# Kernel tuning notes

Measured on AMD Instinct MI355X. Metric: run time of the kernel, lower is better.

## Reference

```python
import jax, jax.numpy as jnp
import numpy as np
import math

L = 4          # num_layers
NH = 8         # num_heads
EPS = 1e-5


def _mha(x, Wqkv, bqkv, Wo, bo):
    # x: (S, B, D). Faithful to torch nn.MultiheadAttention (eval mode).
    S, B, D = x.shape
    hd = D // NH
    qkv = jnp.einsum('sbd,ed->sbe', x, Wqkv) + bqkv            # (S,B,3D)
    q, k, v = jnp.split(qkv, 3, axis=-1)
    def heads(t):
        return t.reshape(S, B, NH, hd).transpose(1, 2, 0, 3)   # (B,H,S,hd)
    q, k, v = heads(q), heads(k), heads(v)
    scale = 1.0 / math.sqrt(hd)
    att = jax.nn.softmax(jnp.einsum('bhqd,bhkd->bhqk', q * scale, k), axis=-1)
    o = jnp.einsum('bhqk,bhkd->bhqd', att, v)                  # (B,H,S,hd)
    o = o.transpose(2, 0, 1, 3).reshape(S, B, D)
    return o @ Wo.T + bo


def _layer_norm(x, g, b):
    mu = jnp.mean(x, axis=-1, keepdims=True)
    var = jnp.var(x, axis=-1, keepdims=True)
    return (x - mu) / jnp.sqrt(var + EPS) * g + b


def _pos_encoding(S, D, dtype):
    pos = jnp.arange(S, dtype=jnp.float32)[:, None]
    div = jnp.exp(jnp.arange(0, D, 2, dtype=jnp.float32) * (-math.log(10000.0) / D))
    pe = jnp.stack([jnp.sin(pos * div), jnp.cos(pos * div)], axis=-1).reshape(S, D)
    return pe.astype(dtype)


def setup_inputs() -> dict:
    key = jax.random.key(0)
    B, S, IN, D, OUT = 8, 2048, 14, 512, 1
    FF = 4 * D
    ks = iter(jax.random.split(key, 32))
    s = 0.02
    inp = {
        'x': jax.random.normal(next(ks), (B, S, IN), jnp.float32),
        'W_emb': jax.random.normal(next(ks), (D, IN), jnp.float32) * s,
        'b_emb': jnp.zeros((D,), jnp.float32),
        'Wqkv_g': jax.random.normal(next(ks), (L, 3 * D, D), jnp.float32) * s,
        'bqkv_g': jnp.zeros((L, 3 * D), jnp.float32),
        'Wo_g': jax.random.normal(next(ks), (L, D, D), jnp.float32) * s,
        'bo_g': jnp.zeros((L, D), jnp.float32),
        'Wqkv_l': jax.random.normal(next(ks), (L, 3 * D, D), jnp.float32) * s,
        'bqkv_l': jnp.zeros((L, 3 * D), jnp.float32),
        'Wo_l': jax.random.normal(next(ks), (L, D, D), jnp.float32) * s,
        'bo_l': jnp.zeros((L, D), jnp.float32),
        'W1': jax.random.normal(next(ks), (L, FF, D), jnp.float32) * s,
        'b1f': jnp.zeros((L, FF), jnp.float32),
        'W2': jax.random.normal(next(ks), (L, D, FF), jnp.float32) * s,
        'b2f': jnp.zeros((L, D), jnp.float32),
        'g1': jnp.ones((L, D), jnp.float32),
        'be1': jnp.zeros((L, D), jnp.float32),
        'g2': jnp.ones((L, D), jnp.float32),
        'be2': jnp.zeros((L, D), jnp.float32),
        'W_out': jax.random.normal(next(ks), (OUT, D), jnp.float32) * s,
        'b_out': jnp.zeros((OUT,), jnp.float32),
    }
    return inp


def reference(x, W_emb, b_emb, Wqkv_g, bqkv_g, Wo_g, bo_g, Wqkv_l, bqkv_l,
              Wo_l, bo_l, W1, b1f, W2, b2f, g1, be1, g2, be2, W_out, b_out):
    B, S, _ = x.shape
    D = W_emb.shape[0]
    h = x @ W_emb.T + b_emb                       # (B,S,D)
    h = h + _pos_encoding(S, D, h.dtype)[None]
    h = h.transpose(1, 0, 2)                      # (S,B,D)

    w = max(1, S // 4)                            # local window size
    nw = S // w                                   # S divisible by w here
    for i in range(L):
        g_out = _mha(h, Wqkv_g[i], bqkv_g[i], Wo_g[i], bo_g[i])
        # local windows: fold window index into batch (attention is per-batch)
        xl = h.reshape(nw, w, B, D).transpose(1, 0, 2, 3).reshape(w, nw * B, D)
        l_out = _mha(xl, Wqkv_l[i], bqkv_l[i], Wo_l[i], bo_l[i])
        l_out = l_out.reshape(w, nw, B, D).transpose(1, 0, 2, 3).reshape(S, B, D)
        h = _layer_norm(h + g_out + l_out, g1[i], be1[i])
        ff = jax.nn.relu(h @ W1[i].T + b1f[i]) @ W2[i].T + b2f[i]
        h = _layer_norm(h + ff, g2[i], be2[i])

    return h[-1] @ W_out.T + b_out                # (B, output_dim)
```

## Files before the change

kernel.cpp:

```cpp
#include <hip/hip_runtime.h>
#include <hip/hip_bf16.h>

#define DEV __device__ __forceinline__

typedef __attribute__((ext_vector_type(4))) float f32x4;
typedef __attribute__((ext_vector_type(8))) short s16x8;
typedef unsigned short u16;

constexpr int Bsz = 8;
constexpr int S   = 2048;
constexpr int Dm  = 512;
constexpr int NHd = 8;
constexpr int FFd = 2048;
constexpr int Ln  = 4;
constexpr int T   = S * Bsz;

DEV u16 f2bf(float f) {
  union { float f; unsigned u; } v; v.f = f;
  unsigned r = v.u + 0x7fff + ((v.u >> 16) & 1);
  return (u16)(r >> 16);
}
DEV float bf2f(u16 a) { union { unsigned u; float f; } v; v.u = ((unsigned)a) << 16; return v.f; }
DEV float exp2g(float x) { return __builtin_amdgcn_exp2f(x); }

typedef __attribute__((address_space(1))) const unsigned int guint;
typedef __attribute__((address_space(3))) unsigned int luint;
DEV void gload16(const void* g, void* l) {
  __builtin_amdgcn_global_load_lds((guint*)g, (luint*)l, 16, 0, 0);
}

__global__ void cvt_bf16_kernel(const float* __restrict__ src, u16* __restrict__ dst, int n4) {
  int i = (blockIdx.x * 256 + threadIdx.x);
  if (i >= n4) return;
  float4 v = *reinterpret_cast<const float4*>(src + i * 4);
  ushort4 o; o.x = f2bf(v.x); o.y = f2bf(v.y); o.z = f2bf(v.z); o.w = f2bf(v.w);
  *reinterpret_cast<ushort4*>(dst + i * 4) = o;
}

__global__ void cvt_wo_kernel(const float* __restrict__ g, const float* __restrict__ l,
                              u16* __restrict__ dst) {
  int i = blockIdx.x * 256 + threadIdx.x;
  int e = i * 4;
  int li = e >> 19;
  int rem = e & 524287;
  int n = rem >> 10, k = rem & 1023;
  const float* src = (k < 512) ? (g + ((size_t)li * 512 + n) * 512 + k)
                               : (l + ((size_t)li * 512 + n) * 512 + (k - 512));
  float4 v = *reinterpret_cast<const float4*>(src);
  ushort4 o; o.x = f2bf(v.x); o.y = f2bf(v.y); o.z = f2bf(v.z); o.w = f2bf(v.w);
  *reinterpret_cast<ushort4*>(dst + e) = o;
}

__global__ void embed_kernel(const float* __restrict__ x, const float* __restrict__ Wemb,
                             const float* __restrict__ bemb, float* __restrict__ hf,
                             u16* __restrict__ hb) {
  int t = blockIdx.x;
  int b = t >> 11, s = t & 2047;
  const float* xr = x + ((size_t)b * S + s) * 14;
  float xv[14];
  #pragma unroll
  for (int i = 0; i < 14; i++) xv[i] = xr[i];
  for (int d = threadIdx.x; d < Dm; d += blockDim.x) {
    const float* wr = Wemb + d * 14;
    float acc = bemb[d];
    #pragma unroll
    for (int i = 0; i < 14; i++) acc += xv[i] * wr[i];
    float ang = (float)s * expf((float)((d >> 1) * 2) * (-9.210340371976184f / 512.0f));
    acc += (d & 1) ? cosf(ang) : sinf(ang);
    hf[(size_t)t * Dm + d] = acc;
    hb[(size_t)t * Dm + d] = f2bf(acc);
  }
}

template<int OMODE, int VPACK, int BSUM>
__global__ __launch_bounds__(256, 2)
void gemm_bt_kernel(const u16* __restrict__ A, const u16* __restrict__ Bt,
                    const float* __restrict__ bias1, const float* __restrict__ bias2,
                    void* __restrict__ Cout, u16* __restrict__ vpk,
                    int M, int N, int K) {
  __shared__ __align__(16) u16 As[2][128 * 32];
  __shared__ __align__(16) u16 Bs[2][128 * 32];
  const int tid = threadIdx.x;
  const int lane = tid & 63, w = tid >> 6;
  const int wr = w >> 1, wc = w & 1;
  const int lr = lane & 15, lg = lane >> 4;
  const int m0 = blockIdx.y * 128, n0 = blockIdx.x * 128;

  f32x4 acc[4][4] = {};

  const int c1 = tid, c2 = tid + 256;
  const u16* gA1 = A + (size_t)(m0 + (c1 >> 2)) * K + (c1 & 3) * 8;
  const u16* gA2 = A + (size_t)(m0 + (c2 >> 2)) * K + (c2 & 3) * 8;
  const u16* gB1 = Bt + (size_t)(n0 + (c1 >> 2)) * K + (c1 & 3) * 8;
  const u16* gB2 = Bt + (size_t)(n0 + (c2 >> 2)) * K + (c2 & 3) * 8;

  const int nk = K >> 5;
  auto stage = [&](int t, int c) {
    const int kt = t * 32;
    gload16(gA1 + kt, As[c] + c1 * 8); gload16(gA2 + kt, As[c] + c2 * 8);
    gload16(gB1 + kt, Bs[c] + c1 * 8); gload16(gB2 + kt, Bs[c] + c2 * 8);
  };

  stage(0, 0);
  for (int t = 0; t < nk; ++t) {
    const int c = t & 1;
    if (t + 1 < nk) {
      stage(t + 1, c ^ 1);
      asm volatile("s_waitcnt vmcnt(4)" ::: "memory");
    } else {
      asm volatile("s_waitcnt vmcnt(0)" ::: "memory");
    }
    __builtin_amdgcn_s_barrier();

    s16x8 a[4], bb[4];
    #pragma unroll
    for (int i = 0; i < 4; i++) {
      a[i]  = *reinterpret_cast<const s16x8*>(As[c] + ((wr * 64 + i * 16 + lr) * 32 + lg * 8));
      bb[i] = *reinterpret_cast<const s16x8*>(Bs[c] + ((wc * 64 + i * 16 + lr) * 32 + lg * 8));
    }
    #pragma unroll
    for (int mi = 0; mi < 4; mi++)
      #pragma unroll
      for (int ni = 0; ni < 4; ni++)
        acc[mi][ni] = __builtin_amdgcn_mfma_f32_16x16x32_bf16(a[mi], bb[ni], acc[mi][ni], 0, 0, 0);

    __builtin_amdgcn_s_barrier();
  }

  const int sec = VPACK ? (n0 >> 9) : 0;
  const bool isv = VPACK && (sec == 2 || sec == 5);
  const int ldc = VPACK ? 2048 : N;
  const int csub = (VPACK && sec >= 3) ? 512 : 0;
  u16* vdst = nullptr;
  if (isv) vdst = vpk + (sec == 5 ? 8388608 : 0);

  #pragma unroll
  for (int mi = 0; mi < 4; mi++) {
    int row = m0 + wr * 64 + mi * 16 + lg * 4;
    #pragma unroll
    for (int ni = 0; ni < 4; ni++) {
      int col = n0 + wc * 64 + ni * 16 + lr;
      float bv;
      if (VPACK)      bv = (col < 1536) ? bias1[col] : bias2[col - 1536];
      else if (BSUM)  bv = bias1[col] + bias2[col];
      else            bv = bias1[col];
      if (isv) {
        int vcol = col - (sec == 2 ? 1024 : 2560);
        int hh = vcol >> 6, dd = vcol & 63;
        int bb2 = row >> 11, ss = row & 2047;
        ushort4 o;
        o.x = f2bf(acc[mi][ni][0] + bv);
        o.y = f2bf(acc[mi][ni][1] + bv);
        o.z = f2bf(acc[mi][ni][2] + bv);
        o.w = f2bf(acc[mi][ni][3] + bv);
        *reinterpret_cast<ushort4*>(vdst + ((size_t)(bb2 * NHd + hh) * 64 + dd) * S + ss) = o;
      } else {
        #pragma unroll
        for (int r = 0; r < 4; r++) {
          float v = acc[mi][ni][r] + bv;
          if (OMODE == 2) v = v > 0.f ? v : 0.f;
          ((u16*)Cout)[(size_t)(row + r) * ldc + (col - csub)] = f2bf(v);
        }
      }
    }
  }
}

__global__ __launch_bounds__(256, 3)
void flash_kernel(const u16* __restrict__ qkv, const u16* __restrict__ v_pk,
                  u16* __restrict__ ctx, int S_att, int nqb, int qoff, int koff, int coff) {
  const int tid = threadIdx.x;
  const int lane = tid & 63, w = tid >> 6;
  const int lr = lane & 15, lg = lane >> 4;
  const int bid = blockIdx.x;
  const int h = bid & 7;
  const int r_ = bid >> 3;
  const int qb = r_ % nqb;
  const int cw = r_ / nqb;
  const int b = cw & 7, n = cw >> 3;
  const int s_base = n * S_att;
  const int q0A = qb * 128 + w * 16;
  const int q0B = q0A + 64;

  __shared__ __align__(16) u16 KT[2][4096];
  __shared__ __align__(16) u16 VT[2][4096];
  __shared__ __align__(16) u16 p_lds_all[4][16][72];
  u16 (*p_lds)[72] = p_lds_all[w];

  const u16* vbase = v_pk + (size_t)(b * NHd + h) * 64 * S + s_base;

  s16x8 qfA[2], qfB[2];
  {
    const float qs = 0.18033688011112042f;
    const u16* qpA = qkv + ((size_t)b * S + s_base + q0A + lr) * 2048 + qoff + h * 64 + lg * 8;
    const u16* qpB = qkv + ((size_t)b * S + s_base + q0B + lr) * 2048 + qoff + h * 64 + lg * 8;
    s16x8 a0 = *reinterpret_cast<const s16x8*>(qpA);
    s16x8 a1 = *reinterpret_cast<const s16x8*>(qpA + 32);
    s16x8 b0 = *reinterpret_cast<const s16x8*>(qpB);
    s16x8 b1 = *reinterpret_cast<const s16x8*>(qpB + 32);
    #pragma unroll
    for (int j = 0; j < 8; j++) {
      qfA[0][j] = (short)f2bf(bf2f((u16)a0[j]) * qs);
      qfA[1][j] = (short)f2bf(bf2f((u16)a1[j]) * qs);
      qfB[0][j] = (short)f2bf(bf2f((u16)b0[j]) * qs);
      qfB[1][j] = (short)f2bf(bf2f((u16)b1[j]) * qs);
    }
  }

  s16x8 ones;
  #pragma unroll
  for (int j = 0; j < 8; j++) ones[j] = (short)0x3F80;

  float mA = -1e30f, mB = -1e30f;
  f32x4 laccA = (f32x4){0.f, 0.f, 0.f, 0.f}, laccB = (f32x4){0.f, 0.f, 0.f, 0.f};
  f32x4 oaccA[4], oaccB[4];
  #pragma unroll
  for (int nt = 0; nt < 4; nt++) {
    oaccA[nt] = (f32x4){0.f, 0.f, 0.f, 0.f};
    oaccB[nt] = (f32x4){0.f, 0.f, 0.f, 0.f};
  }

  const int seg = tid & 7, sr1 = tid >> 3, sr2 = (tid >> 3) + 32;
  const int ssw1 = (seg ^ (sr1 & 7)) * 8, ssw2 = (seg ^ (sr2 & 7)) * 8;

  const u16* kroot = qkv + ((size_t)b * S + s_base) * 2048 + koff + h * 64;

  auto stage = [&](int kb, int c) {
    const u16* kt = kroot + (size_t)kb * 2048;
    gload16(kt + (size_t)sr1 * 2048 + ssw1, &KT[c][tid * 8]);
    gload16(kt + (size_t)sr2 * 2048 + ssw2, &KT[c][2048 + tid * 8]);
    const u16* vt = vbase + kb;
    gload16(vt + (size_t)sr1 * S + ssw1, &VT[c][tid * 8]);
    gload16(vt + (size_t)sr2 * S + ssw2, &VT[c][2048 + tid * 8]);
  };

  stage(0, 0);
  __syncthreads();

  for (int kb = 0; kb < S_att; kb += 64) {
    const int c = (kb >> 6) & 1;
    if (kb + 64 < S_att) stage(kb + 64, c ^ 1);

    f32x4 sgA[4], sgB[4];
    __builtin_amdgcn_s_setprio(1);
    #pragma unroll
    for (int g = 0; g < 4; g++) {
      const int key = g * 16 + lr, kw = key & 7;
      const u16* kp = &KT[c][key * 64];
      s16x8 k0 = *reinterpret_cast<const s16x8*>(kp + ((lg ^ kw) * 8));
      s16x8 k1 = *reinterpret_cast<const s16x8*>(kp + (((4 + lg) ^ kw) * 8));
      f32x4 sa = (f32x4){0.f, 0.f, 0.f, 0.f};
      sa = __builtin_amdgcn_mfma_f32_16x16x32_bf16(k0, qfA[0], sa, 0, 0, 0);
      sa = __builtin_amdgcn_mfma_f32_16x16x32_bf16(k1, qfA[1], sa, 0, 0, 0);
      sgA[g] = sa;
      f32x4 sb = (f32x4){0.f, 0.f, 0.f, 0.f};
      sb = __builtin_amdgcn_mfma_f32_16x16x32_bf16(k0, qfB[0], sb, 0, 0, 0);
      sb = __builtin_amdgcn_mfma_f32_16x16x32_bf16(k1, qfB[1], sb, 0, 0, 0);
      sgB[g] = sb;
    }
    __builtin_amdgcn_s_setprio(0);

    float tmA, tmB;
    {
      float t0 = fmaxf(fmaxf(sgA[0][0], sgA[0][1]), fmaxf(sgA[0][2], sgA[0][3]));
      float t1 = fmaxf(fmaxf(sgA[1][0], sgA[1][1]), fmaxf(sgA[1][2], sgA[1][3]));
      float t2 = fmaxf(fmaxf(sgA[2][0], sgA[2][1]), fmaxf(sgA[2][2], sgA[2][3]));
      float t3 = fmaxf(fmaxf(sgA[3][0], sgA[3][1]), fmaxf(sgA[3][2], sgA[3][3]));
      tmA = fmaxf(fmaxf(t0, t1), fmaxf(t2, t3));
      tmA = fmaxf(tmA, __shfl_xor(tmA, 16, 64));
      tmA = fmaxf(tmA, __shfl_xor(tmA, 32, 64));
      float u0 = fmaxf(fmaxf(sgB[0][0], sgB[0][1]), fmaxf(sgB[0][2], sgB[0][3]));
      float u1 = fmaxf(fmaxf(sgB[1][0], sgB[1][1]), fmaxf(sgB[1][2], sgB[1][3]));
      float u2 = fmaxf(fmaxf(sgB[2][0], sgB[2][1]), fmaxf(sgB[2][2], sgB[2][3]));
      float u3 = fmaxf(fmaxf(sgB[3][0], sgB[3][1]), fmaxf(sgB[3][2], sgB[3][3]));
      tmB = fmaxf(fmaxf(u0, u1), fmaxf(u2, u3));
      tmB = fmaxf(tmB, __shfl_xor(tmB, 16, 64));
      tmB = fmaxf(tmB, __shfl_xor(tmB, 32, 64));
    }
    if (__any((int)(tmA > mA + 8.f))) {
      float mnew = fmaxf(mA, tmA);
      float cf = exp2g(mA - mnew);
      mA = mnew;
      #pragma unroll
      for (int r = 0; r < 4; r++) {
        float co = __shfl(cf, lg * 4 + r, 16);
        laccA[r] *= co;
        #pragma unroll
        for (int nt = 0; nt < 4; nt++) oaccA[nt][r] *= co;
      }
    }
    if (__any((int)(tmB > mB + 8.f))) {
      float mnew = fmaxf(mB, tmB);
      float cf = exp2g(mB - mnew);
      mB = mnew;
      #pragma unroll
      for (int r = 0; r < 4; r++) {
        float co = __shfl(cf, lg * 4 + r, 16);
        laccB[r] *= co;
        #pragma unroll
        for (int nt = 0; nt < 4; nt++) oaccB[nt][r] *= co;
      }
    }

    asm volatile("s_waitcnt lgkmcnt(0)" ::: "memory");
    #pragma unroll
    for (int g = 0; g < 4; g++) {
      float e0 = exp2g(sgA[g][0] - mA);
      float e1 = exp2g(sgA[g][1] - mA);
      float e2 = exp2g(sgA[g][2] - mA);
      float e3 = exp2g(sgA[g][3] - mA);
      unsigned p01, p23;
      asm("v_cvt_pk_bf16_f32 %0, %1, %2" : "=v"(p01) : "v"(e0), "v"(e1));
      asm("v_cvt_pk_bf16_f32 %0, %1, %2" : "=v"(p23) : "v"(e2), "v"(e3));
      uint2 pk; pk.x = p01; pk.y = p23;
      *reinterpret_cast<uint2*>(&p_lds[lr][g * 16 + lg * 4]) = pk;
    }
    asm volatile("s_waitcnt lgkmcnt(0)" ::: "memory");

    __builtin_amdgcn_s_setprio(1);
    #pragma unroll
    for (int kc = 0; kc < 2; kc++) {
      s16x8 pa = *reinterpret_cast<const s16x8*>(&p_lds[lr][kc * 32 + lg * 8]);
      laccA = __builtin_amdgcn_mfma_f32_16x16x32_bf16(pa, ones, laccA, 0, 0, 0);
      #pragma unroll
      for (int nt = 0; nt < 4; nt++) {
        const int d = nt * 16 + lr;
        s16x8 vfr = *reinterpret_cast<const s16x8*>(
            &VT[c][d * 64 + (((kc * 4 + lg) ^ (d & 7)) * 8)]);
        oaccA[nt] = __builtin_amdgcn_mfma_f32_16x16x32_bf16(pa, vfr, oaccA[nt], 0, 0, 0);
      }
    }
    __builtin_amdgcn_s_setprio(0);

    asm volatile("s_waitcnt lgkmcnt(0)" ::: "memory");
    #pragma unroll
    for (int g = 0; g < 4; g++) {
      float e0 = exp2g(sgB[g][0] - mB);
      float e1 = exp2g(sgB[g][1] - mB);
      float e2 = exp2g(sgB[g][2] - mB);
      float e3 = exp2g(sgB[g][3] - mB);
      unsigned p01, p23;
      asm("v_cvt_pk_bf16_f32 %0, %1, %2" : "=v"(p01) : "v"(e0), "v"(e1));
      asm("v_cvt_pk_bf16_f32 %0, %1, %2" : "=v"(p23) : "v"(e2), "v"(e3));
      uint2 pk; pk.x = p01; pk.y = p23;
      *reinterpret_cast<uint2*>(&p_lds[lr][g * 16 + lg * 4]) = pk;
    }
    asm volatile("s_waitcnt lgkmcnt(0)" ::: "memory");

    __builtin_amdgcn_s_setprio(1);
    #pragma unroll
    for (int kc = 0; kc < 2; kc++) {
      s16x8 pa = *reinterpret_cast<const s16x8*>(&p_lds[lr][kc * 32 + lg * 8]);
      laccB = __builtin_amdgcn_mfma_f32_16x16x32_bf16(pa, ones, laccB, 0, 0, 0);
      #pragma unroll
      for (int nt = 0; nt < 4; nt++) {
        const int d = nt * 16 + lr;
        s16x8 vfr = *reinterpret_cast<const s16x8*>(
            &VT[c][d * 64 + (((kc * 4 + lg) ^ (d & 7)) * 8)]);
        oaccB[nt] = __builtin_amdgcn_mfma_f32_16x16x32_bf16(pa, vfr, oaccB[nt], 0, 0, 0);
      }
    }
    __builtin_amdgcn_s_setprio(0);

    __syncthreads();
  }

  #pragma unroll
  for (int nt = 0; nt < 4; nt++)
    #pragma unroll
    for (int r = 0; r < 4; r++) {
      float vA = oaccA[nt][r] / laccA[r];
      size_t tqA = (size_t)b * S + s_base + q0A + lg * 4 + r;
      ctx[tqA * 1024 + coff + h * 64 + nt * 16 + lr] = f2bf(vA);
      float vB = oaccB[nt][r] / laccB[r];
      size_t tqB = (size_t)b * S + s_base + q0B + lg * 4 + r;
      ctx[tqB * 1024 + coff + h * 64 + nt * 16 + lr] = f2bf(vB);
    }
}

template<int NADD>
__global__ void ln_kernel(const float* __restrict__ hin, const u16* __restrict__ a1,
                          const u16* __restrict__ a2, const float* __restrict__ gamma,
                          const float* __restrict__ beta, float* __restrict__ hf,
                          u16* __restrict__ hb) {
  int row = blockIdx.x * 4 + (threadIdx.x >> 6);
  int lane = threadIdx.x & 63;
  size_t base = (size_t)row * 512 + lane * 8;
  float4 h0 = *reinterpret_cast<const float4*>(hin + base);
  float4 h1 = *reinterpret_cast<const float4*>(hin + base + 4);
  s16x8 x1 = *reinterpret_cast<const s16x8*>(a1 + base);
  s16x8 x2 = {};
  if (NADD == 2) x2 = *reinterpret_cast<const s16x8*>(a2 + base);
  float v[8];
  float hv[8] = {h0.x, h0.y, h0.z, h0.w, h1.x, h1.y, h1.z, h1.w};
  float sum = 0.f;
  #pragma unroll
  for (int j = 0; j < 8; j++) {
    float t = hv[j] + bf2f((u16)x1[j]);
    if (NADD == 2) t += bf2f((u16)x2[j]);
    v[j] = t; sum += t;
  }
  #pragma unroll
  for (int o = 32; o >= 1; o >>= 1) sum += __shfl_xor(sum, o, 64);
  float mean = sum * (1.0f / 512.0f);
  float sq = 0.f;
  #pragma unroll
  for (int j = 0; j < 8; j++) { float d = v[j] - mean; sq += d * d; }
  #pragma unroll
  for (int o = 32; o >= 1; o >>= 1) sq += __shfl_xor(sq, o, 64);
  float rstd = rsqrtf(sq * (1.0f / 512.0f) + 1e-5f);
  #pragma unroll
  for (int j = 0; j < 8; j++) {
    int d = lane * 8 + j;
    float o = (v[j] - mean) * rstd * gamma[d] + beta[d];
    hf[base + j] = o;
    hb[base + j] = f2bf(o);
  }
}

__global__ void out_kernel(const float* __restrict__ hf, const float* __restrict__ Wout,
                           const float* __restrict__ bout, float* __restrict__ out) {
  int b = blockIdx.x; int lane = threadIdx.x;
  size_t base = ((size_t)b * S + S - 1) * 512;
  float s = 0.f;
  #pragma unroll
  for (int j = 0; j < 8; j++) { int d = lane * 8 + j; s += hf[base + d] * Wout[d]; }
  #pragma unroll
  for (int o = 32; o >= 1; o >>= 1) s += __shfl_xor(s, o, 64);
  if (lane == 0) out[b] = s + bout[0];
}

extern "C" void kernel_launch(void* const* d_in, const int* in_sizes, int n_in,
                              void* d_out, int out_size, void* d_ws, size_t ws_size,
                              hipStream_t stream) {
  (void)in_sizes; (void)n_in; (void)out_size; (void)ws_size;
  const float* x      = (const float*)d_in[0];
  const float* W_emb  = (const float*)d_in[1];
  const float* b_emb  = (const float*)d_in[2];
  const float* Wqkv_g = (const float*)d_in[3];
  const float* bqkv_g = (const float*)d_in[4];
  const float* Wo_g   = (const float*)d_in[5];
  const float* bo_g   = (const float*)d_in[6];
  const float* Wqkv_l = (const float*)d_in[7];
  const float* bqkv_l = (const float*)d_in[8];
  const float* Wo_l   = (const float*)d_in[9];
  const float* bo_l   = (const float*)d_in[10];
  const float* W1     = (const float*)d_in[11];
  const float* b1f    = (const float*)d_in[12];
  const float* W2     = (const float*)d_in[13];
  const float* b2f    = (const float*)d_in[14];
  const float* g1     = (const float*)d_in[15];
  const float* be1    = (const float*)d_in[16];
  const float* g2     = (const float*)d_in[17];
  const float* be2    = (const float*)d_in[18];
  const float* W_out  = (const float*)d_in[19];
  const float* b_out  = (const float*)d_in[20];
  float* out = (float*)d_out;

  char* ws = (char*)d_ws;
  u16*   w_bf = (u16*)ws;
  float* h_f  = (float*)(ws + 33554432);
  u16*   h_b  = (u16*)(ws + 67108864);
  u16*   qkv  = (u16*)(ws + 83886080);
  u16*   ff1  = (u16*)(ws + 83886080);
  u16*   vpk  = (u16*)(ws + 150994944);
  u16*   ctx  = (u16*)(ws + 184549376);
  u16*   go   = (u16*)(ws + 218103808);

  u16* wqkvF = w_bf;
  u16* woF   = w_bf + 6291456;
  u16* w1b   = w_bf + 8388608;
  u16* w2b   = w_bf + 12582912;

  auto cvt = [&](const float* s_, u16* d_, int n) {
    cvt_bf16_kernel<<<(n / 4 + 255) / 256, 256, 0, stream>>>(s_, d_, n / 4);
  };
  for (int i = 0; i < Ln; i++) {
    cvt(Wqkv_g + (size_t)i * 786432, wqkvF + (size_t)i * 1572864, 786432);
    cvt(Wqkv_l + (size_t)i * 786432, wqkvF + (size_t)i * 1572864 + 786432, 786432);
  }
  cvt_wo_kernel<<<2048, 256, 0, stream>>>(Wo_g, Wo_l, woF);
  cvt(W1, w1b, 4194304);
  cvt(W2, w2b, 4194304);

  embed_kernel<<<T, 256, 0, stream>>>(x, W_emb, b_emb, h_f, h_b);

  for (int i = 0; i < Ln; i++) {
    gemm_bt_kernel<1, 1, 0><<<dim3(3072 / 128, T / 128), 256, 0, stream>>>(
        h_b, wqkvF + (size_t)i * 1572864, bqkv_g + i * 1536, bqkv_l + i * 1536,
        qkv, vpk, T, 3072, 512);
    flash_kernel<<<dim3(1024), 256, 0, stream>>>(qkv, vpk, ctx, 2048, 16, 0, 512, 0);
    flash_kernel<<<dim3(1024), 256, 0, stream>>>(qkv, vpk + 8388608, ctx, 512, 4, 1024, 1536, 512);
    gemm_bt_kernel<1, 0, 1><<<dim3(512 / 128, T / 128), 256, 0, stream>>>(
        ctx, woF + (size_t)i * 524288, bo_g + i * 512, bo_l + i * 512,
        go, nullptr, T, 512, 1024);
    ln_kernel<1><<<T / 4, 256, 0, stream>>>(h_f, go, nullptr, g1 + i * 512, be1 + i * 512, h_f, h_b);
    gemm_bt_kernel<2, 0, 0><<<dim3(FFd / 128, T / 128), 256, 0, stream>>>(
        h_b, w1b + (size_t)i * 1048576, b1f + i * 2048, nullptr, ff1, nullptr, T, 2048, 512);
    gemm_bt_kernel<1, 0, 0><<<dim3(512 / 128, T / 128), 256, 0, stream>>>(
        ff1, w2b + (size_t)i * 1048576, b2f + i * 512, nullptr, go, nullptr, T, 512, 2048);
    ln_kernel<1><<<T / 4, 256, 0, stream>>>(h_f, go, nullptr, g2 + i * 512, be2 + i * 512, h_f, h_b);
  }

  out_kernel<<<Bsz, 64, 0, stream>>>(h_f, W_out, b_out, out);
}
```

Measured before the change: 1.659 ms.

## Merge global and local flash launches, interleave A/B PV MFMAs, raise GEMM occupancy

The global and local attention launches are merged into one 2048-block flash kernel that picks its parameters from the block index, so the tail of each launch no longer leaves the GPU partly idle. Inside the kernel, the A and B P tiles go to separate LDS buffers, which lets both exp/convert phases run back to back and then issue their PV MFMAs together under one wait, removing two lgkmcnt waits per iteration. Separately, GEMM launch bounds rise from 2 to 3 waves per SIMD, which may force register spills. The extra P buffer raises flash LDS use, which could limit occupancy.

```diff
diff --git a/kernel.cpp b/kernel.cpp
--- a/kernel.cpp
+++ b/kernel.cpp
@@ -73,7 +73,7 @@
 }
 
 template<int OMODE, int VPACK, int BSUM>
-__global__ __launch_bounds__(256, 2)
+__global__ __launch_bounds__(256, 3)
 void gemm_bt_kernel(const u16* __restrict__ A, const u16* __restrict__ Bt,
                     const float* __restrict__ bias1, const float* __restrict__ bias2,
                     void* __restrict__ Cout, u16* __restrict__ vpk,
@@ -167,25 +167,34 @@
 }
 
 __global__ __launch_bounds__(256, 3)
-void flash_kernel(const u16* __restrict__ qkv, const u16* __restrict__ v_pk,
-                  u16* __restrict__ ctx, int S_att, int nqb, int qoff, int koff, int coff) {
+void flash_kernel(const u16* __restrict__ qkv, const u16* __restrict__ vpk_all,
+                  u16* __restrict__ ctx) {
   const int tid = threadIdx.x;
   const int lane = tid & 63, w = tid >> 6;
   const int lr = lane & 15, lg = lane >> 4;
   const int bid = blockIdx.x;
-  const int h = bid & 7;
-  const int r_ = bid >> 3;
-  const int qb = r_ % nqb;
-  const int cw = r_ / nqb;
+  const int half = bid >> 10;
+  const int bid10 = bid & 1023;
+  const int h = bid10 & 7;
+  const int r_ = bid10 >> 3;
+  const int S_att = half ? 512 : 2048;
+  const int lognqb = half ? 2 : 4;
+  const int qb = r_ & ((1 << lognqb) - 1);
+  const int cw = r_ >> lognqb;
   const int b = cw & 7, n = cw >> 3;
+  const int qoff = half ? 1024 : 0;
+  const int koff = half ? 1536 : 512;
+  const int coff = half ? 512 : 0;
+  const u16* v_pk = vpk_all + (half ? 8388608 : 0);
   const int s_base = n * S_att;
   const int q0A = qb * 128 + w * 16;
   const int q0B = q0A + 64;
 
   __shared__ __align__(16) u16 KT[2][4096];
   __shared__ __align__(16) u16 VT[2][4096];
-  __shared__ __align__(16) u16 p_lds_all[4][16][72];
-  u16 (*p_lds)[72] = p_lds_all[w];
+  __shared__ __align__(16) u16 p_lds_all[4][2][16][72];
+  u16 (*p_ldsA)[72] = p_lds_all[w][0];
+  u16 (*p_ldsB)[72] = p_lds_all[w][1];
 
   const u16* vbase = v_pk + (size_t)(b * NHd + h) * 64 * S + s_base;
 
@@ -302,7 +311,6 @@
       }
     }
 
-    asm volatile("s_waitcnt lgkmcnt(0)" ::: "memory");
     #pragma unroll
     for (int g = 0; g < 4; g++) {
       float e0 = exp2g(sgA[g][0] - mA);
@@ -313,26 +321,8 @@
       asm("v_cvt_pk_bf16_f32 %0, %1, %2" : "=v"(p01) : "v"(e0), "v"(e1));
       asm("v_cvt_pk_bf16_f32 %0, %1, %2" : "=v"(p23) : "v"(e2), "v"(e3));
       uint2 pk; pk.x = p01; pk.y = p23;
-      *reinterpret_cast<uint2*>(&p_lds[lr][g * 16 + lg * 4]) = pk;
-    }
-    asm volatile("s_waitcnt lgkmcnt(0)" ::: "memory");
-
-    __builtin_amdgcn_s_setprio(1);
-    #pragma unroll
-    for (int kc = 0; kc < 2; kc++) {
-      s16x8 pa = *reinterpret_cast<const s16x8*>(&p_lds[lr][kc * 32 + lg * 8]);
-      laccA = __builtin_amdgcn_mfma_f32_16x16x32_bf16(pa, ones, laccA, 0, 0, 0);
-      #pragma unroll
-      for (int nt = 0; nt < 4; nt++) {
-        const int d = nt * 16 + lr;
-        s16x8 vfr = *reinterpret_cast<const s16x8*>(
-            &VT[c][d * 64 + (((kc * 4 + lg) ^ (d & 7)) * 8)]);
-        oaccA[nt] = __builtin_amdgcn_mfma_f32_16x16x32_bf16(pa, vfr, oaccA[nt], 0, 0, 0);
-      }
-    }
-    __builtin_amdgcn_s_setprio(0);
-
-    asm volatile("s_waitcnt lgkmcnt(0)" ::: "memory");
+      *reinterpret_cast<uint2*>(&p_ldsA[lr][g * 16 + lg * 4]) = pk;
+    }
     #pragma unroll
     for (int g = 0; g < 4; g++) {
       float e0 = exp2g(sgB[g][0] - mB);
@@ -343,21 +333,24 @@
       asm("v_cvt_pk_bf16_f32 %0, %1, %2" : "=v"(p01) : "v"(e0), "v"(e1));
       asm("v_cvt_pk_bf16_f32 %0, %1, %2" : "=v"(p23) : "v"(e2), "v"(e3));
       uint2 pk; pk.x = p01; pk.y = p23;
-      *reinterpret_cast<uint2*>(&p_lds[lr][g * 16 + lg * 4]) = pk;
+      *reinterpret_cast<uint2*>(&p_ldsB[lr][g * 16 + lg * 4]) = pk;
     }
     asm volatile("s_waitcnt lgkmcnt(0)" ::: "memory");
 
     __builtin_amdgcn_s_setprio(1);
     #pragma unroll
     for (int kc = 0; kc < 2; kc++) {
-      s16x8 pa = *reinterpret_cast<const s16x8*>(&p_lds[lr][kc * 32 + lg * 8]);
-      laccB = __builtin_amdgcn_mfma_f32_16x16x32_bf16(pa, ones, laccB, 0, 0, 0);
+      s16x8 paA = *reinterpret_cast<const s16x8*>(&p_ldsA[lr][kc * 32 + lg * 8]);
+      s16x8 paB = *reinterpret_cast<const s16x8*>(&p_ldsB[lr][kc * 32 + lg * 8]);
+      laccA = __builtin_amdgcn_mfma_f32_16x16x32_bf16(paA, ones, laccA, 0, 0, 0);
+      laccB = __builtin_amdgcn_mfma_f32_16x16x32_bf16(paB, ones, laccB, 0, 0, 0);
       #pragma unroll
       for (int nt = 0; nt < 4; nt++) {
         const int d = nt * 16 + lr;
         s16x8 vfr = *reinterpret_cast<const s16x8*>(
             &VT[c][d * 64 + (((kc * 4 + lg) ^ (d & 7)) * 8)]);
-        oaccB[nt] = __builtin_amdgcn_mfma_f32_16x16x32_bf16(pa, vfr, oaccB[nt], 0, 0, 0);
+        oaccA[nt] = __builtin_amdgcn_mfma_f32_16x16x32_bf16(paA, vfr, oaccA[nt], 0, 0, 0);
+        oaccB[nt] = __builtin_amdgcn_mfma_f32_16x16x32_bf16(paB, vfr, oaccB[nt], 0, 0, 0);
       }
     }
     __builtin_amdgcn_s_setprio(0);
@@ -489,8 +482,7 @@
     gemm_bt_kernel<1, 1, 0><<<dim3(3072 / 128, T / 128), 256, 0, stream>>>(
         h_b, wqkvF + (size_t)i * 1572864, bqkv_g + i * 1536, bqkv_l + i * 1536,
         qkv, vpk, T, 3072, 512);
-    flash_kernel<<<dim3(1024), 256, 0, stream>>>(qkv, vpk, ctx, 2048, 16, 0, 512, 0);
-    flash_kernel<<<dim3(1024), 256, 0, stream>>>(qkv, vpk + 8388608, ctx, 512, 4, 1024, 1536, 512);
+    flash_kernel<<<dim3(2048), 256, 0, stream>>>(qkv, vpk, ctx);
     gemm_bt_kernel<1, 0, 1><<<dim3(512 / 128, T / 128), 256, 0, stream>>>(
         ctx, woF + (size_t)i * 524288, bo_g + i * 512, bo_l + i * 512,
         go, nullptr, T, 512, 1024);
```

New measurement: 1.548 ms. 6.7% less time.
